# Kernel optimization log

Hardware: AMD Instinct MI355X
Metric: run time of the kernel (lower is better)

The kernel has to match this reference:

```python
import jax, jax.numpy as jnp
import numpy as np

N, E, F, H, S, L, B = 20000, 320000, 64, 256, 32, 128, 16
TAU = 1.0
EPS = 1e-9


def _glorot(k, i, o):
    return (jax.random.normal(k, (i, o), jnp.float32) / np.sqrt(i)).astype(jnp.float32)


def _mlp3(h, w1, b1, w2, b2, w3, b3):
    h = jax.nn.relu(h @ w1 + b1)
    h = jax.nn.relu(h @ w2 + b2)
    return h @ w3 + b3


def _gnn_layer(x, src, dst, w1, b1, w2, b2, w3, b3):
    # PyG: x_i = x[dst] (target), x_j = x[src] (source); aggregate 'add' at target
    m = _mlp3(jnp.concatenate([x[dst], x[src]], axis=1), w1, b1, w2, b2, w3, b3)  # [E, H]
    return jax.ops.segment_sum(m, dst, num_segments=N)  # [N, H]


def _layer_norm(x, g, b):
    mu = x.mean(-1, keepdims=True)
    var = ((x - mu) ** 2).mean(-1, keepdims=True)
    return (x - mu) * jax.lax.rsqrt(var + 1e-5) * g + b


def setup_inputs() -> dict:
    key = jax.random.key(0)
    ks = jax.random.split(key, 32)
    d = {
        'x': jax.random.normal(ks[0], (N, F), jnp.float32),
        'u': jax.random.uniform(ks[1], (N, S), jnp.float32, minval=1e-6, maxval=1.0 - 1e-6),
        'edge_index': jax.random.randint(ks[2], (2, E), 0, N, jnp.int32),
        'batch': jnp.sort(jax.random.randint(ks[3], (N,), 0, B, jnp.int32)),
        # gnn1 MLP: 2F -> H -> H -> H
        'g1w1': _glorot(ks[4], 2 * F, H), 'g1b1': jnp.zeros((H,), jnp.float32),
        'g1w2': _glorot(ks[5], H, H),     'g1b2': jnp.zeros((H,), jnp.float32),
        'g1w3': _glorot(ks[6], H, H),     'g1b3': jnp.zeros((H,), jnp.float32),
        'ln1g': jnp.ones((H,), jnp.float32), 'ln1b': jnp.zeros((H,), jnp.float32),
        # gnn2 MLP: 2H -> H -> H -> H
        'g2w1': _glorot(ks[7], 2 * H, H), 'g2b1': jnp.zeros((H,), jnp.float32),
        'g2w2': _glorot(ks[8], H, H),     'g2b2': jnp.zeros((H,), jnp.float32),
        'g2w3': _glorot(ks[9], H, H),     'g2b3': jnp.zeros((H,), jnp.float32),
        'ln2g': jnp.ones((H,), jnp.float32), 'ln2b': jnp.zeros((H,), jnp.float32),
        # assignment MLP: H -> H -> S
        'aw1': _glorot(ks[10], H, H), 'ab1': jnp.zeros((H,), jnp.float32),
        'aw2': _glorot(ks[11], H, S), 'ab2': jnp.zeros((S,), jnp.float32),
        # output MLP: H -> H -> L
        'ow1': _glorot(ks[12], H, H), 'ob1': jnp.zeros((H,), jnp.float32),
        'ow2': _glorot(ks[13], H, L), 'ob2': jnp.zeros((L,), jnp.float32),
    }
    return d


def reference(x, u, edge_index, batch,
              g1w1, g1b1, g1w2, g1b2, g1w3, g1b3, ln1g, ln1b,
              g2w1, g2b1, g2w2, g2b2, g2w3, g2b3, ln2g, ln2b,
              aw1, ab1, aw2, ab2, ow1, ob1, ow2, ob2):
    src, dst = edge_index[0], edge_index[1]
    x = _layer_norm(jax.nn.relu(_gnn_layer(x, src, dst, g1w1, g1b1, g1w2, g1b2, g1w3, g1b3)), ln1g, ln1b)
    x = _layer_norm(jax.nn.relu(_gnn_layer(x, src, dst, g2w1, g2b1, g2w2, g2b2, g2w3, g2b3)), ln2g, ln2b)
    # Hierarchical pooling with Gumbel-softmax (soft, tau=1.0); u is the uniform noise
    logits = jax.nn.relu(x @ aw1 + ab1) @ aw2 + ab2  # [N, S]
    g = -jnp.log(-jnp.log(u + EPS) + EPS)
    s = jax.nn.softmax((logits + g) / TAU, axis=-1)  # [N, S]
    entropy = -jnp.mean(jnp.sum(s * jnp.log(s + EPS), axis=1))
    avg_s = s.mean(axis=0)
    diversity = jnp.sum(avg_s * jnp.log(avg_s + EPS))
    assign_loss = entropy + diversity
    xe = x[:, None, :] * s[:, :, None]  # [N, S, H]
    pooled = jax.ops.segment_sum(xe, batch, num_segments=B)  # [B, S, H]
    latent = jax.nn.relu(pooled @ ow1 + ob1) @ ow2 + ob2  # [B, S, L]
    return (latent, s, assign_loss)
```

## Files before the change

kernel.cpp:

```cpp
#include <hip/hip_runtime.h>
#include <stdint.h>

#define NN 20000
#define NE 320000
#define NBATCH 16
#define NTILE 2500

typedef short short8 __attribute__((ext_vector_type(8)));
typedef float f32x4  __attribute__((ext_vector_type(4)));

__device__ __forceinline__ unsigned short f2bf(float f) {
  union { float f; unsigned u; } v; v.f = f;
  unsigned r = v.u + 0x7FFFu + ((v.u >> 16) & 1u);
  return (unsigned short)(r >> 16);
}
__device__ __forceinline__ float bf2f(unsigned short h) {
  union { unsigned u; float f; } v; v.u = ((unsigned)h) << 16;
  return v.f;
}
__device__ __forceinline__ float bf2fs(short h) { return bf2f((unsigned short)h); }

__device__ __forceinline__ unsigned cvt_pk_bf16(float lo, float hi) {
  unsigned r;
  asm("v_cvt_pk_bf16_f32 %0, %1, %2" : "=v"(r) : "v"(lo), "v"(hi));
  return r;
}

#define HOFF(e, k) (((e) << 8) + (((((k) >> 3) ^ ((e) & 7)) << 3) + ((k) & 7)))
#define HK(e, k, KT) ((e) * (KT) + (((((k) >> 3) ^ ((e) & 7)) << 3) + ((k) & 7)))

struct TD { const float* s; unsigned short* d; int R, C, r0, ld; };
struct TDs { TD t[13]; };

__global__ void wprep(TDs all, const int* __restrict__ dstI, int* __restrict__ deg) {
  if (blockIdx.y == 13) {
    int stride = gridDim.x * blockDim.x;
    for (int e = blockIdx.x * blockDim.x + threadIdx.x; e < NE; e += stride)
      atomicAdd(&deg[dstI[e]], 1);
    return;
  }
  TD td = all.t[blockIdx.y];
  int stride = gridDim.x * blockDim.x;
  int i0 = blockIdx.x * blockDim.x + threadIdx.x;
  if (td.ld == 0) {
    for (int i = i0; i < td.R; i += stride) td.d[i] = f2bf(td.s[i]);
  } else {
    int total = td.R * td.C;
    for (int i = i0; i < total; i += stride) {
      int c = i / td.R;
      int r = i - c * td.R;
      td.d[i] = f2bf(td.s[(size_t)(td.r0 + r) * td.ld + c]);
    }
  }
}

__global__ void scan_bounds(const int* __restrict__ deg, int* __restrict__ rowstart,
                            int* __restrict__ cursor, const int* __restrict__ batch,
                            int* __restrict__ bstart,
                            const float* __restrict__ g1b1, const float* __restrict__ g2b1,
                            float* __restrict__ b1cat1, float* __restrict__ b1cat2) {
  if (blockIdx.x == 0) {
    __shared__ int part[256];
    int t = threadIdx.x;
    int c0 = t * 80; if (c0 > NN) c0 = NN;
    int c1 = c0 + 80; if (c1 > NN) c1 = NN;
    int s = 0;
    for (int i = c0; i < c1; ++i) s += deg[i];
    part[t] = s;
    __syncthreads();
    if (t == 0) {
      int run = 0;
      for (int i = 0; i < 256; ++i) { int v = part[i]; part[i] = run; run += v; }
    }
    __syncthreads();
    int run = part[t];
    for (int i = c0; i < c1; ++i) { rowstart[i] = run; cursor[i] = run; run += deg[i]; }
    if (t == 255) rowstart[NN] = run;
  } else if (blockIdx.x == 80) {
    int t = threadIdx.x;
    b1cat1[t] = g1b1[t]; b1cat1[256 + t] = 0.f;
    b1cat2[t] = g2b1[t]; b1cat2[256 + t] = 0.f;
  } else {
    int n = (blockIdx.x - 1) * 256 + threadIdx.x;
    if (n >= NN) return;
    int bn = batch[n];
    if (n == 0) {
      for (int b2 = 0; b2 <= bn; ++b2) bstart[b2] = 0;
    } else {
      int bp = batch[n - 1];
      for (int b2 = bp + 1; b2 <= bn; ++b2) bstart[b2] = n;
    }
    if (n == NN - 1) {
      for (int b2 = bn + 1; b2 <= NBATCH; ++b2) bstart[b2] = NN;
    }
  }
}

__global__ void fillcsr(const int* __restrict__ srcI, const int* __restrict__ dstI,
                        int* __restrict__ cursor, int* __restrict__ sSrc,
                        int* __restrict__ sDst) {
  int e = blockIdx.x * 256 + threadIdx.x;
  if (e < NE) {
    int d = dstI[e];
    int slot = atomicAdd(&cursor[d], 1);
    sDst[slot] = d;
    sSrc[slot] = srcI[e];
  }
}

template <int KT>
__global__ __launch_bounds__(512, 2) void gemmTs(
    const unsigned short* __restrict__ WT, const unsigned short* __restrict__ In,
    const float* __restrict__ bias, unsigned short* __restrict__ Out,
    int M, int Nout, int ldo) {
  __shared__ __align__(16) unsigned short h[128 * KT];
  const int tid = threadIdx.x;
  const int rb0 = blockIdx.y * 128;
  {
    int r = tid & 127;
    int rg = rb0 + r; if (rg >= M) rg = M - 1;
    const unsigned short* src = In + (size_t)rg * KT + (tid >> 7) * (KT / 4);
    int c0 = (tid >> 7) * (KT / 4);
#pragma unroll
    for (int i = 0; i < KT / 32; ++i) {
      short8 v = *(const short8*)(src + i * 8);
      *(short8*)&h[HK(r, c0 + i * 8, KT)] = v;
    }
  }
  __syncthreads();

  const int lane = tid & 63, w = tid >> 6;
  const int wf = w >> 1, we = w & 1;
  const int l15 = lane & 15, q = lane >> 4;
  const int fb = blockIdx.x * 256 + wf * 64;
  const int rb = rb0 + we * 64;
  f32x4 acc[4][4] = {};
  const short8 zz = {0, 0, 0, 0, 0, 0, 0, 0};
  for (int kc = 0; kc < KT; kc += 32) {
    short8 a[4], bq[4];
#pragma unroll
    for (int i = 0; i < 4; ++i) {
      if (fb + i * 16 < Nout)
        a[i] = *(const short8*)(WT + (size_t)(fb + i * 16 + l15) * KT + kc + q * 8);
      else
        a[i] = zz;
      bq[i] = *(const short8*)&h[HK(we * 64 + i * 16 + l15, kc + q * 8, KT)];
    }
#pragma unroll
    for (int i = 0; i < 4; ++i)
#pragma unroll
      for (int j = 0; j < 4; ++j)
        acc[i][j] = __builtin_amdgcn_mfma_f32_16x16x32_bf16(a[i], bq[j], acc[i][j], 0, 0, 0);
  }
#pragma unroll
  for (int i = 0; i < 4; ++i) {
    int f0 = fb + i * 16 + q * 4;
    if (f0 >= Nout) continue;
    float4 bs = make_float4(0.f, 0.f, 0.f, 0.f);
    if (bias) bs = *(const float4*)(bias + f0);
#pragma unroll
    for (int j = 0; j < 4; ++j) {
      int r = rb + j * 16 + l15;
      if (r >= M) continue;
      uint2 o = make_uint2(cvt_pk_bf16(acc[i][j][0] + bs.x, acc[i][j][1] + bs.y),
                           cvt_pk_bf16(acc[i][j][2] + bs.z, acc[i][j][3] + bs.w));
      *(uint2*)(Out + (size_t)r * ldo + f0) = o;
    }
  }
}

__global__ __launch_bounds__(512, 2) void edge_h2agg(
    const unsigned short* __restrict__ PQ, const int* __restrict__ sSrc,
    const int* __restrict__ sDst,
    const unsigned short* __restrict__ W2T, const float* __restrict__ b2,
    float* __restrict__ agg) {
  __shared__ __align__(16) unsigned short h[128 * 256];
  __shared__ int seg_s[129];
  const int tid = threadIdx.x;
  const int e0 = blockIdx.x * 128;
  if (tid == 0) seg_s[128] = 0;

  {
    int r = tid & 127;
    int c0 = (tid >> 7) * 64;
    int dn = sDst[e0 + r];
    int sn = sSrc[e0 + r];
    const unsigned short* pd = PQ + (size_t)dn * 512 + c0;
    const unsigned short* ps = PQ + (size_t)sn * 512 + 256 + c0;
#pragma unroll
    for (int i = 0; i < 8; ++i) {
      short8 dv = *(const short8*)(pd + i * 8);
      short8 sv = *(const short8*)(ps + i * 8);
      float a0 = fmaxf(bf2fs(dv[0]) + bf2fs(sv[0]), 0.f);
      float a1 = fmaxf(bf2fs(dv[1]) + bf2fs(sv[1]), 0.f);
      float a2 = fmaxf(bf2fs(dv[2]) + bf2fs(sv[2]), 0.f);
      float a3 = fmaxf(bf2fs(dv[3]) + bf2fs(sv[3]), 0.f);
      float a4 = fmaxf(bf2fs(dv[4]) + bf2fs(sv[4]), 0.f);
      float a5 = fmaxf(bf2fs(dv[5]) + bf2fs(sv[5]), 0.f);
      float a6 = fmaxf(bf2fs(dv[6]) + bf2fs(sv[6]), 0.f);
      float a7 = fmaxf(bf2fs(dv[7]) + bf2fs(sv[7]), 0.f);
      uint4 o = make_uint4(cvt_pk_bf16(a0, a1), cvt_pk_bf16(a2, a3),
                           cvt_pk_bf16(a4, a5), cvt_pk_bf16(a6, a7));
      *(uint4*)&h[HOFF(r, c0 + i * 8)] = o;
    }
  }
  __syncthreads();

  const int lane = tid & 63, w = tid >> 6;
  const int wf = w >> 1, we = w & 1;
  const int l15 = lane & 15, q = lane >> 4;
  const int fb = wf * 64, eb = we * 64;
  f32x4 acc[4][4];

#pragma unroll
  for (int i = 0; i < 4; ++i)
#pragma unroll
    for (int j = 0; j < 4; ++j) { f32x4 z = {0.f, 0.f, 0.f, 0.f}; acc[i][j] = z; }
  for (int kc = 0; kc < 256; kc += 32) {
    short8 a[4], bq[4];
#pragma unroll
    for (int i = 0; i < 4; ++i)
      a[i] = *(const short8*)(W2T + (size_t)(fb + i * 16 + l15) * 256 + kc + q * 8);
#pragma unroll
    for (int j = 0; j < 4; ++j)
      bq[j] = *(const short8*)&h[HOFF(eb + j * 16 + l15, kc + q * 8)];
#pragma unroll
    for (int i = 0; i < 4; ++i)
#pragma unroll
      for (int j = 0; j < 4; ++j)
        acc[i][j] = __builtin_amdgcn_mfma_f32_16x16x32_bf16(a[i], bq[j], acc[i][j], 0, 0, 0);
  }
  __syncthreads();
#pragma unroll
  for (int i = 0; i < 4; ++i) {
    int f0 = fb + i * 16 + q * 4;
    float4 bs = *(const float4*)(b2 + f0);
#pragma unroll
    for (int j = 0; j < 4; ++j) {
      int e = eb + j * 16 + l15;
      float v0 = fmaxf(acc[i][j][0] + bs.x, 0.f);
      float v1 = fmaxf(acc[i][j][1] + bs.y, 0.f);
      float v2 = fmaxf(acc[i][j][2] + bs.z, 0.f);
      float v3 = fmaxf(acc[i][j][3] + bs.w, 0.f);
      uint2 o = make_uint2(cvt_pk_bf16(v0, v1), cvt_pk_bf16(v2, v3));
      *(uint2*)&h[HOFF(e, f0)] = o;
    }
  }
  if (tid < 128) {
    int d0 = sDst[e0 + tid];
    bool flag = (tid == 0) || (sDst[e0 + tid - 1] != d0);
    if (flag) {
      int idx = atomicAdd(&seg_s[128], 1);
      seg_s[idx] = tid;
    }
  }
  __syncthreads();

  {
    int cnt = seg_s[128];
    int f4 = (tid & 63) * 4;
    int sg = tid >> 6;
    for (int k = sg; k < cnt; k += 8) {
      int start = seg_s[k];
      int end = 128;
      for (int j2 = 0; j2 < cnt; ++j2) {
        int v = seg_s[j2];
        if (v > start && v < end) end = v;
      }
      int node = sDst[e0 + start];
      float s0 = 0.f, s1 = 0.f, s2 = 0.f, s3 = 0.f;
      for (int rr = start; rr < end; ++rr) {
        ushort4 v = *(const ushort4*)&h[HOFF(rr, f4)];
        s0 += bf2f(v.x); s1 += bf2f(v.y); s2 += bf2f(v.z); s3 += bf2f(v.w);
      }
      float* pr = agg + (size_t)node * 256 + f4;
      if (start == 0 || end == 128) {
        atomicAdd(pr + 0, s0); atomicAdd(pr + 1, s1);
        atomicAdd(pr + 2, s2); atomicAdd(pr + 3, s3);
      } else {
        *(float4*)pr = make_float4(s0, s1, s2, s3);
      }
    }
  }
}

__global__ __launch_bounds__(512, 2) void node_gemm(
    const unsigned short* __restrict__ W3T, const float* __restrict__ aggH2,
    const float* __restrict__ b3, const int* __restrict__ deg,
    float* __restrict__ outm) {
  __shared__ __align__(16) unsigned short h[128 * 256];
  const int tid = threadIdx.x;
  const int rb0 = blockIdx.x * 128;
  {
    int r = tid & 127;
    int rg = rb0 + r; if (rg >= NN) rg = NN - 1;
    int c0 = (tid >> 7) * 64;
    const float* src = aggH2 + (size_t)rg * 256 + c0;
#pragma unroll
    for (int i = 0; i < 8; ++i) {
      float4 lo = *(const float4*)(src + i * 8);
      float4 hi = *(const float4*)(src + i * 8 + 4);
      uint4 o = make_uint4(cvt_pk_bf16(lo.x, lo.y), cvt_pk_bf16(lo.z, lo.w),
                           cvt_pk_bf16(hi.x, hi.y), cvt_pk_bf16(hi.z, hi.w));
      *(uint4*)&h[HOFF(r, c0 + i * 8)] = o;
    }
  }
  __syncthreads();

  const int lane = tid & 63, w = tid >> 6;
  const int wf = w >> 1, we = w & 1;
  const int l15 = lane & 15, q = lane >> 4;
  const int fb = wf * 64;
  const int rb = rb0 + we * 64;
  f32x4 acc[4][4] = {};
  for (int kc = 0; kc < 256; kc += 32) {
    short8 a[4], bq[4];
#pragma unroll
    for (int i = 0; i < 4; ++i) {
      a[i] = *(const short8*)(W3T + (size_t)(fb + i * 16 + l15) * 256 + kc + q * 8);
      bq[i] = *(const short8*)&h[HOFF(we * 64 + i * 16 + l15, kc + q * 8)];
    }
#pragma unroll
    for (int i = 0; i < 4; ++i)
#pragma unroll
      for (int j = 0; j < 4; ++j)
        acc[i][j] = __builtin_amdgcn_mfma_f32_16x16x32_bf16(a[i], bq[j], acc[i][j], 0, 0, 0);
  }
#pragma unroll
  for (int i = 0; i < 4; ++i) {
    int f0 = fb + i * 16 + q * 4;
    float4 b3v = *(const float4*)(b3 + f0);
#pragma unroll
    for (int j = 0; j < 4; ++j) {
      int r = rb + j * 16 + l15;
      if (r >= NN) continue;
      float dg = (float)deg[r];
      *(float4*)(outm + (size_t)r * 256 + f0) =
          make_float4(acc[i][j][0] + dg * b3v.x, acc[i][j][1] + dg * b3v.y,
                      acc[i][j][2] + dg * b3v.z, acc[i][j][3] + dg * b3v.w);
    }
  }
}

__global__ void relu_ln(const float* __restrict__ agg, const float* __restrict__ g,
                        const float* __restrict__ b, unsigned short* __restrict__ out) {
  int row = blockIdx.x * 4 + (threadIdx.x >> 6);
  int lane = threadIdx.x & 63;
  if (row >= NN) return;
  float4 v = *(const float4*)(agg + (size_t)row * 256 + lane * 4);
  v.x = fmaxf(v.x, 0.f); v.y = fmaxf(v.y, 0.f); v.z = fmaxf(v.z, 0.f); v.w = fmaxf(v.w, 0.f);
  float s = v.x + v.y + v.z + v.w;
  float sq = v.x * v.x + v.y * v.y + v.z * v.z + v.w * v.w;
  for (int off = 32; off >= 1; off >>= 1) {
    s += __shfl_xor(s, off);
    sq += __shfl_xor(sq, off);
  }
  float mu = s * (1.f / 256.f);
  float var = sq * (1.f / 256.f) - mu * mu;
  float rs = rsqrtf(var + 1e-5f);
  float4 gg = *(const float4*)(g + lane * 4);
  float4 bb = *(const float4*)(b + lane * 4);
  ushort4 o;
  o.x = f2bf((v.x - mu) * rs * gg.x + bb.x);
  o.y = f2bf((v.y - mu) * rs * gg.y + bb.y);
  o.z = f2bf((v.z - mu) * rs * gg.z + bb.z);
  o.w = f2bf((v.w - mu) * rs * gg.w + bb.w);
  *(ushort4*)(out + (size_t)row * 256 + lane * 4) = o;
}

__global__ __launch_bounds__(512, 4) void assign_gumbel(
    const unsigned short* __restrict__ x2b, const unsigned short* __restrict__ aw1T,
    const float* __restrict__ ab1, const unsigned short* __restrict__ aw2T,
    const float* __restrict__ ab2, const float* __restrict__ u,
    float* __restrict__ sf, float* __restrict__ entacc, float* __restrict__ avgacc) {
  __shared__ __align__(16) unsigned short sh[64 * 256];
  __shared__ float sh_logit[64 * 33];
  __shared__ float lavg[32];
  __shared__ float lent;
  const int tid = threadIdx.x;
  const int n0 = blockIdx.x * 64;
  if (tid < 32) lavg[tid] = 0.f;
  if (tid == 0) lent = 0.f;

  const int lane = tid & 63, w = tid >> 6;
  const int l15 = lane & 15, q = lane >> 4;

  {
    const int wf = w >> 1, we = w & 1;
    const int fb = wf * 64, eb = we * 32;
    f32x4 acc[4][2];
#pragma unroll
    for (int i = 0; i < 4; ++i)
#pragma unroll
      for (int j = 0; j < 2; ++j) { f32x4 z = {0.f, 0.f, 0.f, 0.f}; acc[i][j] = z; }
    for (int kc = 0; kc < 256; kc += 32) {
      short8 a[4], bq[2];
#pragma unroll
      for (int i = 0; i < 4; ++i)
        a[i] = *(const short8*)(aw1T + (size_t)(fb + i * 16 + l15) * 256 + kc + q * 8);
#pragma unroll
      for (int j = 0; j < 2; ++j) {
        int rr = n0 + eb + j * 16 + l15;
        if (rr >= NN) rr = NN - 1;
        bq[j] = *(const short8*)(x2b + (size_t)rr * 256 + kc + q * 8);
      }
#pragma unroll
      for (int i = 0; i < 4; ++i)
#pragma unroll
        for (int j = 0; j < 2; ++j)
          acc[i][j] = __builtin_amdgcn_mfma_f32_16x16x32_bf16(a[i], bq[j], acc[i][j], 0, 0, 0);
    }
#pragma unroll
    for (int i = 0; i < 4; ++i) {
      int f0 = fb + i * 16 + q * 4;
      float4 bs = *(const float4*)(ab1 + f0);
#pragma unroll
      for (int j = 0; j < 2; ++j) {
        int e = eb + j * 16 + l15;
        ushort4 o;
        o.x = f2bf(fmaxf(acc[i][j][0] + bs.x, 0.f));
        o.y = f2bf(fmaxf(acc[i][j][1] + bs.y, 0.f));
        o.z = f2bf(fmaxf(acc[i][j][2] + bs.z, 0.f));
        o.w = f2bf(fmaxf(acc[i][j][3] + bs.w, 0.f));
        *(ushort4*)&sh[HOFF(e, f0)] = o;
      }
    }
  }
  __syncthreads();

  {
    const int rg = w & 3, fg = w >> 2;
    if (fg < 2) {
      f32x4 acc = {0.f, 0.f, 0.f, 0.f};
      for (int kc = 0; kc < 256; kc += 32) {
        short8 a = *(const short8*)(aw2T + (size_t)(fg * 16 + l15) * 256 + kc + q * 8);
        short8 bq = *(const short8*)&sh[HOFF(rg * 16 + l15, kc + q * 8)];
        acc = __builtin_amdgcn_mfma_f32_16x16x32_bf16(a, bq, acc, 0, 0, 0);
      }
      int rowL = rg * 16 + l15;
#pragma unroll
      for (int t2 = 0; t2 < 4; ++t2) {
        int f = fg * 16 + q * 4 + t2;
        sh_logit[rowL * 33 + f] = acc[t2] + ab2[f];
      }
    }
  }
  __syncthreads();

  if (tid < 256) {
    int rowL = tid >> 2, sub = tid & 3;
    int n = n0 + rowL;
    if (n < NN) {
      int j0 = sub * 8;
      float z[8];
      float4 u0 = *(const float4*)(u + (size_t)n * 32 + j0);
      float4 u1 = *(const float4*)(u + (size_t)n * 32 + j0 + 4);
      float uu[8] = {u0.x, u0.y, u0.z, u0.w, u1.x, u1.y, u1.z, u1.w};
      float m = -1e30f;
#pragma unroll
      for (int j = 0; j < 8; ++j) {
        z[j] = sh_logit[rowL * 33 + j0 + j] - logf(-logf(uu[j] + 1e-9f) + 1e-9f);
        m = fmaxf(m, z[j]);
      }
      m = fmaxf(m, __shfl_xor(m, 1));
      m = fmaxf(m, __shfl_xor(m, 2));
      float sum = 0.f;
#pragma unroll
      for (int j = 0; j < 8; ++j) { z[j] = expf(z[j] - m); sum += z[j]; }
      sum += __shfl_xor(sum, 1);
      sum += __shfl_xor(sum, 2);
      float inv = 1.f / sum;
      float ent = 0.f;
      float so[8];
#pragma unroll
      for (int j = 0; j < 8; ++j) {
        float sj = z[j] * inv;
        so[j] = sj;
        ent += sj * logf(sj + 1e-9f);
        atomicAdd(&lavg[j0 + j], sj);
      }
      *(float4*)(sf + (size_t)n * 32 + j0) = make_float4(so[0], so[1], so[2], so[3]);
      *(float4*)(sf + (size_t)n * 32 + j0 + 4) = make_float4(so[4], so[5], so[6], so[7]);
      ent += __shfl_xor(ent, 1);
      ent += __shfl_xor(ent, 2);
      if (sub == 0) atomicAdd(&lent, ent);
    }
  }
  __syncthreads();
  if (tid < 32) atomicAdd(&avgacc[tid], lavg[tid]);
  if (tid == 0) atomicAdd(entacc, lent);
}

__global__ __launch_bounds__(512, 4) void pool_part(
    const unsigned short* __restrict__ x2b, const float* __restrict__ sf,
    const int* __restrict__ bstart, float* __restrict__ part) {
  const int b = blockIdx.x, ci = blockIdx.y;
  const int n0b = bstart[b], n1b = bstart[b + 1];
  const int t = threadIdx.x;
  const int si = t >> 4;
  const int h0 = (t & 15) * 16;
  float acc[16];
#pragma unroll
  for (int k = 0; k < 16; ++k) acc[k] = 0.f;
  for (int nst = n0b + ci * 64; nst < n1b; nst += 16 * 64) {
    int nend = (nst + 64 < n1b) ? nst + 64 : n1b;
    for (int n = nst; n < nend; ++n) {
      float sv = sf[(size_t)n * 32 + si];
      const unsigned short* xr = x2b + (size_t)n * 256 + h0;
      short8 x0 = *(const short8*)xr;
      short8 x1 = *(const short8*)(xr + 8);
#pragma unroll
      for (int j = 0; j < 8; ++j) acc[j] = fmaf(sv, bf2fs(x0[j]), acc[j]);
#pragma unroll
      for (int j = 0; j < 8; ++j) acc[8 + j] = fmaf(sv, bf2fs(x1[j]), acc[8 + j]);
    }
  }
  float* pp = part + (((size_t)b * 16 + ci) << 13) + si * 256 + h0;
#pragma unroll
  for (int k = 0; k < 16; k += 4)
    *(float4*)(pp + k) = make_float4(acc[k], acc[k + 1], acc[k + 2], acc[k + 3]);
}

__global__ void pool_reduce(const float* __restrict__ part, float* __restrict__ pooled) {
  int g = blockIdx.x * 256 + threadIdx.x;
  int b = g >> 13, rem = g & 8191;
  const float* p = part + (((size_t)b * 16) << 13) + rem;
  float s = 0.f;
#pragma unroll
  for (int c = 0; c < 16; ++c) s += p[(size_t)c << 13];
  pooled[g] = s;
}

__global__ __launch_bounds__(512, 4) void out_mlp(
    const float* __restrict__ pooled, const unsigned short* __restrict__ ow1T,
    const float* __restrict__ ob1, const unsigned short* __restrict__ ow2T,
    const float* __restrict__ ob2, float* __restrict__ latent,
    const float* __restrict__ accs, float* __restrict__ outloss) {
  __shared__ __align__(16) unsigned short sh[64 * 256];
  const int tid = threadIdx.x;
  const int n0 = blockIdx.x * 64;
  const int lane = tid & 63, w = tid >> 6;
  const int l15 = lane & 15, q = lane >> 4;

  if (blockIdx.x == 0 && tid < 64) {
    float d = 0.f;
    if (tid < 32) {
      float a = accs[16 + tid] * (1.f / NN);
      d = a * logf(a + 1e-9f);
    }
    for (int off = 32; off >= 1; off >>= 1) d += __shfl_xor(d, off);
    if (tid == 0) outloss[0] = -accs[0] * (1.f / NN) + d;
  }

  {
    const int wf = w >> 1, we = w & 1;
    const int fb = wf * 64, eb = we * 32;
    f32x4 acc[4][2];
#pragma unroll
    for (int i = 0; i < 4; ++i)
#pragma unroll
      for (int j = 0; j < 2; ++j) { f32x4 z = {0.f, 0.f, 0.f, 0.f}; acc[i][j] = z; }
    for (int kc = 0; kc < 256; kc += 32) {
      short8 a[4], bq[2];
#pragma unroll
      for (int i = 0; i < 4; ++i)
        a[i] = *(const short8*)(ow1T + (size_t)(fb + i * 16 + l15) * 256 + kc + q * 8);
#pragma unroll
      for (int j = 0; j < 2; ++j) {
        int rr = n0 + eb + j * 16 + l15;
        const float* pr = pooled + (size_t)rr * 256 + kc + q * 8;
        float4 lo = *(const float4*)pr;
        float4 hi = *(const float4*)(pr + 4);
        short8 o;
        o[0] = (short)f2bf(lo.x); o[1] = (short)f2bf(lo.y);
        o[2] = (short)f2bf(lo.z); o[3] = (short)f2bf(lo.w);
        o[4] = (short)f2bf(hi.x); o[5] = (short)f2bf(hi.y);
        o[6] = (short)f2bf(hi.z); o[7] = (short)f2bf(hi.w);
        bq[j] = o;
      }
#pragma unroll
      for (int i = 0; i < 4; ++i)
#pragma unroll
        for (int j = 0; j < 2; ++j)
          acc[i][j] = __builtin_amdgcn_mfma_f32_16x16x32_bf16(a[i], bq[j], acc[i][j], 0, 0, 0);
    }
#pragma unroll
    for (int i = 0; i < 4; ++i) {
      int f0 = fb + i * 16 + q * 4;
      float4 bs = *(const float4*)(ob1 + f0);
#pragma unroll
      for (int j = 0; j < 2; ++j) {
        int e = eb + j * 16 + l15;
        ushort4 o;
        o.x = f2bf(fmaxf(acc[i][j][0] + bs.x, 0.f));
        o.y = f2bf(fmaxf(acc[i][j][1] + bs.y, 0.f));
        o.z = f2bf(fmaxf(acc[i][j][2] + bs.z, 0.f));
        o.w = f2bf(fmaxf(acc[i][j][3] + bs.w, 0.f));
        *(ushort4*)&sh[HOFF(e, f0)] = o;
      }
    }
  }
  __syncthreads();

  {
    const int wf = w >> 1, we = w & 1;
    const int fb = wf * 32, eb = we * 32;
    f32x4 acc[2][2];
#pragma unroll
    for (int i = 0; i < 2; ++i)
#pragma unroll
      for (int j = 0; j < 2; ++j) { f32x4 z = {0.f, 0.f, 0.f, 0.f}; acc[i][j] = z; }
    for (int kc = 0; kc < 256; kc += 32) {
      short8 a[2], bq[2];
#pragma unroll
      for (int i = 0; i < 2; ++i)
        a[i] = *(const short8*)(ow2T + (size_t)(fb + i * 16 + l15) * 256 + kc + q * 8);
#pragma unroll
      for (int j = 0; j < 2; ++j)
        bq[j] = *(const short8*)&sh[HOFF(eb + j * 16 + l15, kc + q * 8)];
#pragma unroll
      for (int i = 0; i < 2; ++i)
#pragma unroll
        for (int j = 0; j < 2; ++j)
          acc[i][j] = __builtin_amdgcn_mfma_f32_16x16x32_bf16(a[i], bq[j], acc[i][j], 0, 0, 0);
    }
#pragma unroll
    for (int i = 0; i < 2; ++i) {
      int f0 = fb + i * 16 + q * 4;
      float4 bs = *(const float4*)(ob2 + f0);
#pragma unroll
      for (int j = 0; j < 2; ++j) {
        int rr = n0 + eb + j * 16 + l15;
        *(float4*)(latent + (size_t)rr * 128 + f0) =
            make_float4(acc[i][j][0] + bs.x, acc[i][j][1] + bs.y,
                        acc[i][j][2] + bs.z, acc[i][j][3] + bs.w);
      }
    }
  }
}

extern "C" void kernel_launch(void* const* d_in, const int* in_sizes, int n_in,
                              void* d_out, int out_size, void* d_ws, size_t ws_size,
                              hipStream_t stream) {
  (void)in_sizes; (void)n_in; (void)out_size; (void)ws_size;
  const float* x = (const float*)d_in[0];
  const float* u = (const float*)d_in[1];
  const int* ei = (const int*)d_in[2];
  const int* batch = (const int*)d_in[3];
  const float* g1w1 = (const float*)d_in[4];
  const float* g1b1 = (const float*)d_in[5];
  const float* g1w2 = (const float*)d_in[6];
  const float* g1b2 = (const float*)d_in[7];
  const float* g1w3 = (const float*)d_in[8];
  const float* g1b3 = (const float*)d_in[9];
  const float* ln1g = (const float*)d_in[10];
  const float* ln1b = (const float*)d_in[11];
  const float* g2w1 = (const float*)d_in[12];
  const float* g2b1 = (const float*)d_in[13];
  const float* g2w2 = (const float*)d_in[14];
  const float* g2b2 = (const float*)d_in[15];
  const float* g2w3 = (const float*)d_in[16];
  const float* g2b3 = (const float*)d_in[17];
  const float* ln2g = (const float*)d_in[18];
  const float* ln2b = (const float*)d_in[19];
  const float* aw1 = (const float*)d_in[20];
  const float* ab1 = (const float*)d_in[21];
  const float* aw2 = (const float*)d_in[22];
  const float* ab2 = (const float*)d_in[23];
  const float* ow1 = (const float*)d_in[24];
  const float* ob1 = (const float*)d_in[25];
  const float* ow2 = (const float*)d_in[26];
  const float* ob2 = (const float*)d_in[27];
  const int* srcI = ei;
  const int* dstI = ei + NE;

  char* wp = (char*)d_ws;
  size_t off = 0;
  auto alloc = [&](size_t bytes) {
    void* p = wp + off;
    off += (bytes + 255) & ~(size_t)255;
    return p;
  };
  unsigned short* W1catT = (unsigned short*)alloc((size_t)512 * 64 * 2);
  unsigned short* W2catT = (unsigned short*)alloc((size_t)512 * 256 * 2);
  unsigned short* g1w2T = (unsigned short*)alloc((size_t)256 * 256 * 2);
  unsigned short* g1w3T = (unsigned short*)alloc((size_t)256 * 256 * 2);
  unsigned short* g2w2T = (unsigned short*)alloc((size_t)256 * 256 * 2);
  unsigned short* g2w3T = (unsigned short*)alloc((size_t)256 * 256 * 2);
  unsigned short* aw1T = (unsigned short*)alloc((size_t)256 * 256 * 2);
  unsigned short* aw2T = (unsigned short*)alloc((size_t)32 * 256 * 2);
  unsigned short* ow1T = (unsigned short*)alloc((size_t)256 * 256 * 2);
  unsigned short* ow2T = (unsigned short*)alloc((size_t)128 * 256 * 2);
  unsigned short* xb = (unsigned short*)alloc((size_t)NN * 64 * 2);
  unsigned short* PQ = (unsigned short*)alloc((size_t)NN * 512 * 2);
  unsigned short* x1b = (unsigned short*)alloc((size_t)NN * 256 * 2);
  unsigned short* x2b = (unsigned short*)alloc((size_t)NN * 256 * 2);
  int* bstart = (int*)alloc(32 * 4);
  int* cursor = (int*)alloc((size_t)NN * 4);
  int* rowstart = (int*)alloc((size_t)(NN + 1) * 4);
  int* sSrc = (int*)alloc((size_t)NE * 4);
  int* sDst = (int*)alloc((size_t)NE * 4);
  float* b1cat1 = (float*)alloc(512 * 4);
  float* b1cat2 = (float*)alloc(512 * 4);
  char* zbase = (char*)(wp + off);
  float* accs = (float*)alloc(64 * 4);
  float* pooled = (float*)alloc((size_t)512 * 256 * 4);
  int* deg = (int*)alloc((size_t)NN * 4);
  float* agg1 = (float*)alloc((size_t)NN * 256 * 4);
  float* agg2 = (float*)alloc((size_t)NN * 256 * 4);
  size_t zbytes = (size_t)((char*)(wp + off) - zbase);

  float* aggm = (float*)PQ;
  float* poolpart = agg1;

  float* out_f = (float*)d_out;
  float* out_latent = out_f;
  float* out_s = out_f + 65536;
  float* out_loss = out_f + 65536 + 640000;

  TDs tds;
  tds.t[0] = {g1w1, W1catT, 64, 256, 0, 256};
  tds.t[1] = {g1w1, W1catT + 256 * 64, 64, 256, 64, 256};
  tds.t[2] = {g1w2, g1w2T, 256, 256, 0, 256};
  tds.t[3] = {g1w3, g1w3T, 256, 256, 0, 256};
  tds.t[4] = {g2w1, W2catT, 256, 256, 0, 256};
  tds.t[5] = {g2w1, W2catT + 256 * 256, 256, 256, 256, 256};
  tds.t[6] = {g2w2, g2w2T, 256, 256, 0, 256};
  tds.t[7] = {g2w3, g2w3T, 256, 256, 0, 256};
  tds.t[8] = {aw1, aw1T, 256, 256, 0, 256};
  tds.t[9] = {aw2, aw2T, 256, 32, 0, 32};
  tds.t[10] = {ow1, ow1T, 256, 256, 0, 256};
  tds.t[11] = {ow2, ow2T, 256, 128, 0, 128};
  tds.t[12] = {x, xb, NN * 64, 1, 0, 0};

  (void)hipMemsetAsync(zbase, 0, zbytes, stream);
  wprep<<<dim3(128, 14), 256, 0, stream>>>(tds, dstI, deg);

  scan_bounds<<<dim3(81), 256, 0, stream>>>(deg, rowstart, cursor, batch, bstart,
                                            g1b1, g2b1, b1cat1, b1cat2);
  fillcsr<<<dim3(1250), 256, 0, stream>>>(srcI, dstI, cursor, sSrc, sDst);

  gemmTs<64><<<dim3(2, 157), 512, 0, stream>>>(W1catT, xb, b1cat1, PQ, NN, 512, 512);
  edge_h2agg<<<dim3(NTILE), 512, 0, stream>>>(PQ, sSrc, sDst, g1w2T, g1b2, agg1);
  node_gemm<<<dim3(157), 512, 0, stream>>>(g1w3T, agg1, g1b3, deg, aggm);
  relu_ln<<<dim3(5000), 256, 0, stream>>>(aggm, ln1g, ln1b, x1b);

  gemmTs<256><<<dim3(2, 157), 512, 0, stream>>>(W2catT, x1b, b1cat2, PQ, NN, 512, 512);
  edge_h2agg<<<dim3(NTILE), 512, 0, stream>>>(PQ, sSrc, sDst, g2w2T, g2b2, agg2);
  node_gemm<<<dim3(157), 512, 0, stream>>>(g2w3T, agg2, g2b3, deg, aggm);
  relu_ln<<<dim3(5000), 256, 0, stream>>>(aggm, ln2g, ln2b, x2b);

  assign_gumbel<<<dim3(313), 512, 0, stream>>>(x2b, aw1T, ab1, aw2T, ab2, u,
                                               out_s, accs, accs + 16);

  pool_part<<<dim3(16, 16), 512, 0, stream>>>(x2b, out_s, bstart, poolpart);
  pool_reduce<<<dim3(512), 256, 0, stream>>>(poolpart, pooled);

  out_mlp<<<dim3(8), 512, 0, stream>>>(pooled, ow1T, ob1, ow2T, ob2, out_latent,
                                       accs, out_loss);
}
```

Measured before the change: 652.4 us.

## Fuse ReLU+LayerNorm into node GEMM epilogue and tile weight transpose

```diff
diff --git a/kernel.cpp b/kernel.cpp
--- a/kernel.cpp
+++ b/kernel.cpp
@@ -33,6 +33,7 @@
 struct TDs { TD t[13]; };
 
 __global__ void wprep(TDs all, const int* __restrict__ dstI, int* __restrict__ deg) {
+  __shared__ float tile[32][33];
   if (blockIdx.y == 13) {
     int stride = gridDim.x * blockDim.x;
     for (int e = blockIdx.x * blockDim.x + threadIdx.x; e < NE; e += stride)
@@ -40,16 +41,35 @@
     return;
   }
   TD td = all.t[blockIdx.y];
-  int stride = gridDim.x * blockDim.x;
-  int i0 = blockIdx.x * blockDim.x + threadIdx.x;
   if (td.ld == 0) {
-    for (int i = i0; i < td.R; i += stride) td.d[i] = f2bf(td.s[i]);
-  } else {
-    int total = td.R * td.C;
-    for (int i = i0; i < total; i += stride) {
-      int c = i / td.R;
-      int r = i - c * td.R;
-      td.d[i] = f2bf(td.s[(size_t)(td.r0 + r) * td.ld + c]);
+    int stride = gridDim.x * blockDim.x;
+    int n8 = td.R >> 3;
+    for (int i = blockIdx.x * blockDim.x + threadIdx.x; i < n8; i += stride) {
+      const float* s = td.s + (size_t)i * 8;
+      float4 lo = *(const float4*)s;
+      float4 hi = *(const float4*)(s + 4);
+      uint4 o = make_uint4(cvt_pk_bf16(lo.x, lo.y), cvt_pk_bf16(lo.z, lo.w),
+                           cvt_pk_bf16(hi.x, hi.y), cvt_pk_bf16(hi.z, hi.w));
+      *(uint4*)(td.d + (size_t)i * 8) = o;
+    }
+    return;
+  }
+  int tilesR = td.R >> 5, tilesC = td.C >> 5;
+  int nt = tilesR * tilesC;
+  int tr = threadIdx.x >> 5, tc = threadIdx.x & 31;
+  for (int tIdx = blockIdx.x; tIdx < nt; tIdx += gridDim.x) {
+    int t_r = tIdx / tilesC, t_c = tIdx - t_r * tilesC;
+    __syncthreads();
+#pragma unroll
+    for (int rr = 0; rr < 4; ++rr) {
+      int r = t_r * 32 + tr + rr * 8;
+      tile[tr + rr * 8][tc] = td.s[(size_t)(td.r0 + r) * td.ld + t_c * 32 + tc];
+    }
+    __syncthreads();
+#pragma unroll
+    for (int rr = 0; rr < 4; ++rr) {
+      int c = t_c * 32 + tr + rr * 8;
+      td.d[(size_t)c * td.R + t_r * 32 + tc] = f2bf(tile[tc][tr + rr * 8]);
     }
   }
 }
@@ -284,13 +304,16 @@
   }
 }
 
-__global__ __launch_bounds__(512, 2) void node_gemm(
+__global__ __launch_bounds__(512, 2) void node_gemm_ln(
     const unsigned short* __restrict__ W3T, const float* __restrict__ aggH2,
     const float* __restrict__ b3, const int* __restrict__ deg,
-    float* __restrict__ outm) {
+    const float* __restrict__ lng, const float* __restrict__ lnb,
+    unsigned short* __restrict__ out) {
   __shared__ __align__(16) unsigned short h[128 * 256];
+  __shared__ float rstat[256];
   const int tid = threadIdx.x;
   const int rb0 = blockIdx.x * 128;
+  if (tid < 256) rstat[tid] = 0.f;
   {
     int r = tid & 127;
     int rg = rb0 + r; if (rg >= NN) rg = NN - 1;
@@ -326,46 +349,60 @@
       for (int j = 0; j < 4; ++j)
         acc[i][j] = __builtin_amdgcn_mfma_f32_16x16x32_bf16(a[i], bq[j], acc[i][j], 0, 0, 0);
   }
-#pragma unroll
-  for (int i = 0; i < 4; ++i) {
-    int f0 = fb + i * 16 + q * 4;
-    float4 b3v = *(const float4*)(b3 + f0);
-#pragma unroll
-    for (int j = 0; j < 4; ++j) {
-      int r = rb + j * 16 + l15;
-      if (r >= NN) continue;
-      float dg = (float)deg[r];
-      *(float4*)(outm + (size_t)r * 256 + f0) =
-          make_float4(acc[i][j][0] + dg * b3v.x, acc[i][j][1] + dg * b3v.y,
-                      acc[i][j][2] + dg * b3v.z, acc[i][j][3] + dg * b3v.w);
-    }
-  }
-}
-
-__global__ void relu_ln(const float* __restrict__ agg, const float* __restrict__ g,
-                        const float* __restrict__ b, unsigned short* __restrict__ out) {
-  int row = blockIdx.x * 4 + (threadIdx.x >> 6);
-  int lane = threadIdx.x & 63;
-  if (row >= NN) return;
-  float4 v = *(const float4*)(agg + (size_t)row * 256 + lane * 4);
-  v.x = fmaxf(v.x, 0.f); v.y = fmaxf(v.y, 0.f); v.z = fmaxf(v.z, 0.f); v.w = fmaxf(v.w, 0.f);
-  float s = v.x + v.y + v.z + v.w;
-  float sq = v.x * v.x + v.y * v.y + v.z * v.z + v.w * v.w;
-  for (int off = 32; off >= 1; off >>= 1) {
-    s += __shfl_xor(s, off);
-    sq += __shfl_xor(sq, off);
-  }
-  float mu = s * (1.f / 256.f);
-  float var = sq * (1.f / 256.f) - mu * mu;
-  float rs = rsqrtf(var + 1e-5f);
-  float4 gg = *(const float4*)(g + lane * 4);
-  float4 bb = *(const float4*)(b + lane * 4);
-  ushort4 o;
-  o.x = f2bf((v.x - mu) * rs * gg.x + bb.x);
-  o.y = f2bf((v.y - mu) * rs * gg.y + bb.y);
-  o.z = f2bf((v.z - mu) * rs * gg.z + bb.z);
-  o.w = f2bf((v.w - mu) * rs * gg.w + bb.w);
-  *(ushort4*)(out + (size_t)row * 256 + lane * 4) = o;
+
+  float dgj[4];
+#pragma unroll
+  for (int j = 0; j < 4; ++j) {
+    int rr = rb + j * 16 + l15;
+    dgj[j] = (float)deg[rr < NN ? rr : NN - 1];
+  }
+  f32x4 bsv[4];
+#pragma unroll
+  for (int i = 0; i < 4; ++i)
+    bsv[i] = *(const f32x4*)(b3 + fb + i * 16 + q * 4);
+
+#pragma unroll
+  for (int j = 0; j < 4; ++j) {
+    float s = 0.f, sq = 0.f;
+#pragma unroll
+    for (int i = 0; i < 4; ++i)
+#pragma unroll
+      for (int r = 0; r < 4; ++r) {
+        float v = fmaxf(acc[i][j][r] + dgj[j] * bsv[i][r], 0.f);
+        s += v; sq += v * v;
+      }
+    s += __shfl_xor(s, 16); s += __shfl_xor(s, 32);
+    sq += __shfl_xor(sq, 16); sq += __shfl_xor(sq, 32);
+    if (q == 0) {
+      int lr = we * 64 + j * 16 + l15;
+      atomicAdd(&rstat[lr], s);
+      atomicAdd(&rstat[128 + lr], sq);
+    }
+  }
+  __syncthreads();
+
+#pragma unroll
+  for (int j = 0; j < 4; ++j) {
+    int lr = we * 64 + j * 16 + l15;
+    int rr = rb + j * 16 + l15;
+    float mu = rstat[lr] * (1.f / 256.f);
+    float var = rstat[128 + lr] * (1.f / 256.f) - mu * mu;
+    float rs = rsqrtf(var + 1e-5f);
+    if (rr < NN) {
+#pragma unroll
+      for (int i = 0; i < 4; ++i) {
+        int f0 = fb + i * 16 + q * 4;
+        f32x4 gg = *(const f32x4*)(lng + f0);
+        f32x4 bb = *(const f32x4*)(lnb + f0);
+        float o0 = (fmaxf(acc[i][j][0] + dgj[j] * bsv[i][0], 0.f) - mu) * rs * gg[0] + bb[0];
+        float o1 = (fmaxf(acc[i][j][1] + dgj[j] * bsv[i][1], 0.f) - mu) * rs * gg[1] + bb[1];
+        float o2 = (fmaxf(acc[i][j][2] + dgj[j] * bsv[i][2], 0.f) - mu) * rs * gg[2] + bb[2];
+        float o3 = (fmaxf(acc[i][j][3] + dgj[j] * bsv[i][3], 0.f) - mu) * rs * gg[3] + bb[3];
+        *(uint2*)(out + (size_t)rr * 256 + f0) =
+            make_uint2(cvt_pk_bf16(o0, o1), cvt_pk_bf16(o2, o3));
+      }
+    }
+  }
 }
 
 __global__ __launch_bounds__(512, 4) void assign_gumbel(
@@ -710,7 +747,6 @@
   float* agg2 = (float*)alloc((size_t)NN * 256 * 4);
   size_t zbytes = (size_t)((char*)(wp + off) - zbase);
 
-  float* aggm = (float*)PQ;
   float* poolpart = agg1;
 
   float* out_f = (float*)d_out;
@@ -742,13 +778,11 @@
 
   gemmTs<64><<<dim3(2, 157), 512, 0, stream>>>(W1catT, xb, b1cat1, PQ, NN, 512, 512);
   edge_h2agg<<<dim3(NTILE), 512, 0, stream>>>(PQ, sSrc, sDst, g1w2T, g1b2, agg1);
-  node_gemm<<<dim3(157), 512, 0, stream>>>(g1w3T, agg1, g1b3, deg, aggm);
-  relu_ln<<<dim3(5000), 256, 0, stream>>>(aggm, ln1g, ln1b, x1b);
+  node_gemm_ln<<<dim3(157), 512, 0, stream>>>(g1w3T, agg1, g1b3, deg, ln1g, ln1b, x1b);
 
   gemmTs<256><<<dim3(2, 157), 512, 0, stream>>>(W2catT, x1b, b1cat2, PQ, NN, 512, 512);
   edge_h2agg<<<dim3(NTILE), 512, 0, stream>>>(PQ, sSrc, sDst, g2w2T, g2b2, agg2);
-  node_gemm<<<dim3(157), 512, 0, stream>>>(g2w3T, agg2, g2b3, deg, aggm);
-  relu_ln<<<dim3(5000), 256, 0, stream>>>(aggm, ln2g, ln2b, x2b);
+  node_gemm_ln<<<dim3(157), 512, 0, stream>>>(g2w3T, agg2, g2b3, deg, ln2g, ln2b, x2b);
 
   assign_gumbel<<<dim3(313), 512, 0, stream>>>(x2b, aw1T, ab1, aw2T, ab2, u,
                                                out_s, accs, accs + 16);
```

New measurement: 639.5 us. -2.0%, faster.
